# Kernel optimization log

Measured on AMD Instinct MI355X. Metric: run time of the kernel, lower is better.

Reference implementation:

```python
import jax, jax.numpy as jnp
import numpy as np

K_TAPS = 4

def batch_lsigf(h, S, x, b):
    """h: [Gout,E,K,Fin], S: [B,E,N,N], x: [B,Fin,N], b: [Gout,1] -> [B,Gout,N]."""
    Gout, E, K, Fin = h.shape
    B, _, _, N = S.shape
    xk = jnp.broadcast_to(x[:, None], (B, E, Fin, N))  # tap k=0
    taps = [xk]
    for _ in range(1, K):
        xk = jnp.matmul(xk, S)  # [B,E,Fin,N] @ [B,E,N,N]
        taps.append(xk)
    z = jnp.stack(taps, axis=2)  # [B,E,K,Fin,N]
    y = jnp.einsum('bekfn,gekf->bgn', z, h)
    if b is not None:
        y = y + b  # [Gout,1] broadcasts over nodes
    return y

def setup_inputs() -> dict:
    key = jax.random.key(0)
    ks = jax.random.split(key, 9)
    B, N = 16, 1024
    G = F = H = 128
    E, K = 1, K_TAPS
    sa = 1.0 / np.sqrt(G * K)
    sb = 1.0 / np.sqrt(H * K)
    return {
        'x': jax.random.normal(ks[0], (B, G, N), jnp.float32),
        'hidden': jax.random.normal(ks[1], (B, H, N), jnp.float32),
        'S': jax.random.normal(ks[2], (B, E, N, N), jnp.float32) / np.sqrt(N),
        'weight_A': jax.random.uniform(ks[3], (H, E, K, G), jnp.float32, -sa, sa),
        'weight_B': jax.random.uniform(ks[4], (H, E, K, H), jnp.float32, -sb, sb),
        'weight_D': jax.random.uniform(ks[5], (F, E, K, H), jnp.float32, -sb, sb),
        'bias_A': jax.random.uniform(ks[6], (H, 1), jnp.float32, -sa, sa),
        'bias_B': jax.random.uniform(ks[7], (H, 1), jnp.float32, -sb, sb),
        'bias_D': jax.random.uniform(ks[8], (F, 1), jnp.float32, -sb, sb),
    }

def reference(x, hidden, S, weight_A, weight_B, weight_D, bias_A, bias_B, bias_D):
    u_a = batch_lsigf(weight_A, S, x, bias_A)        # input path
    u_b = batch_lsigf(weight_B, S, hidden, bias_B)   # recurrent path
    h_next = jax.nn.relu(u_a + u_b)                  # new hidden state
    u = batch_lsigf(weight_D, S, h_next, bias_D)     # output projection
    return u
```

## Files before the change

kernel.cpp:

```cpp
#include <hip/hip_runtime.h>


typedef __attribute__((ext_vector_type(8))) short short8;
typedef __attribute__((ext_vector_type(4))) float floatx4;

#define AS1 __attribute__((address_space(1)))
#define AS3 __attribute__((address_space(3)))

__device__ __forceinline__ unsigned short f2bf(float f) {
  union { float f; unsigned u; } v; v.f = f;
  unsigned r = v.u + 0x7fffu + ((v.u >> 16) & 1u);
  return (unsigned short)(r >> 16);
}
__device__ __forceinline__ float bf2f(unsigned short b) {
  union { unsigned u; float f; } v; v.u = ((unsigned)b) << 16;
  return v.f;
}

__device__ __forceinline__ void gload16(const void* g, void* l) {
  __builtin_amdgcn_global_load_lds((const AS1 void*)g, (AS3 void*)l, 16, 0, 0);
}

template<int EPI, int KK>
__global__ __launch_bounds__(256, 2)
void gemm_bt(const unsigned short* __restrict__ A, long long aBatch, int lda,
             const unsigned short* __restrict__ Bt, long long bBatch, int ldb,
             const unsigned short* __restrict__ cinit, long long ciBatch,
             const float* __restrict__ bias,
             unsigned short* __restrict__ outb, long long obBatch,
             float* __restrict__ outf, long long ofBatch,
             unsigned short* __restrict__ mixv, long long mvBatch)
{
  constexpr int NT   = KK / 64;
  constexpr int MT   = (EPI == 3) ? 8 : 2;
  constexpr int PERB = 16 * MT;
  __shared__ unsigned short buf[4][128 * 64];

  const int wg  = blockIdx.x;
  const int xcd = wg & 7;
  const int idx = wg >> 3;
  const int b   = xcd * 2 + idx / PERB;
  const int r   = idx % PERB;
  const int n0  = (r & 15) * 64;
  const int m0  = (r >> 4) * 64;

  const int tid  = threadIdx.x;
  const int wave = tid >> 6;
  const int lane = tid & 63;
  const int wr   = (wave >> 1) * 32;
  const int wc   = (wave & 1) * 32;
  const int l15  = lane & 15;
  const int lhi  = lane >> 4;

  const unsigned short* Ab = A + (long long)b * aBatch;
  const unsigned short* Bb = Bt + (long long)b * bBatch;

  const unsigned short* src[4];
  int ldsoff[4];
  #pragma unroll
  for (int i = 0; i < 4; ++i) {
    const int u  = wave * 4 + i;
    const int rr = u * 8 + (lane >> 3);
    const int c8 = ((lane & 7) ^ (rr & 7)) * 8;
    src[i] = (rr < 64) ? Ab + (long long)(m0 + rr) * lda + c8
                       : Bb + (long long)(n0 + rr - 64) * ldb + c8;
    ldsoff[i] = u * 512;
  }
  auto stage = [&](int slot) {
    #pragma unroll
    for (int i = 0; i < 4; ++i) {
      gload16(src[i], &buf[slot][ldsoff[i]]);
      src[i] += 64;
    }
  };

  int aoff[2][2], boff[2][2];
  #pragma unroll
  for (int mi = 0; mi < 2; ++mi)
    #pragma unroll
    for (int kk = 0; kk < 2; ++kk) {
      const int rowa = wr + mi * 16 + l15;
      aoff[kk][mi] = rowa * 64 + (((kk * 4 + lhi) ^ (rowa & 7)) << 3);
      const int rowb = 64 + wc + mi * 16 + l15;
      boff[kk][mi] = rowb * 64 + (((kk * 4 + lhi) ^ (rowb & 7)) << 3);
    }

  floatx4 acc[2][2];
  #pragma unroll
  for (int mi = 0; mi < 2; ++mi)
    #pragma unroll
    for (int ni = 0; ni < 2; ++ni)
      acc[mi][ni] = (floatx4){0.f, 0.f, 0.f, 0.f};

  stage(0);
  if (NT > 1) stage(1);
  if (NT > 2) stage(2);

  #pragma unroll
  for (int t = 0; t < NT; ++t) {
    const int rem = NT - 1 - t;
    if (rem >= 2)      { asm volatile("s_waitcnt vmcnt(8)" ::: "memory"); }
    else if (rem == 1) { asm volatile("s_waitcnt vmcnt(4)" ::: "memory"); }
    else               { asm volatile("s_waitcnt vmcnt(0)" ::: "memory"); }
    __builtin_amdgcn_s_barrier();
    __builtin_amdgcn_sched_barrier(0);
    if (t + 3 < NT) stage((t + 3) & 3);

    const unsigned short* bp = &buf[t & 3][0];
    #pragma unroll
    for (int kk = 0; kk < 2; ++kk) {
      short8 af[2], bv[2];
      #pragma unroll
      for (int mi = 0; mi < 2; ++mi) af[mi] = *(const short8*)(bp + aoff[kk][mi]);
      #pragma unroll
      for (int ni = 0; ni < 2; ++ni) bv[ni] = *(const short8*)(bp + boff[kk][ni]);
      __builtin_amdgcn_s_setprio(1);
      #pragma unroll
      for (int mi = 0; mi < 2; ++mi)
        #pragma unroll
        for (int ni = 0; ni < 2; ++ni)
          acc[mi][ni] = __builtin_amdgcn_mfma_f32_16x16x32_bf16(af[mi], bv[ni], acc[mi][ni], 0, 0, 0);
      __builtin_amdgcn_s_setprio(0);
    }
  }

  if (EPI == 0) {
    const unsigned short* ci = cinit + (long long)b * ciBatch;
    unsigned short* ob = outb + (long long)b * obBatch;
    #pragma unroll
    for (int mi = 0; mi < 2; ++mi)
      #pragma unroll
      for (int ni = 0; ni < 2; ++ni)
        #pragma unroll
        for (int j = 0; j < 4; ++j) {
          const int row = m0 + wr + mi * 16 + lhi * 4 + j;
          const int col = n0 + wc + ni * 16 + l15;
          ob[(long long)row * 1024 + col] =
              f2bf(acc[mi][ni][j] + bf2f(ci[(long long)row * 1024 + col]));
        }
  } else if (EPI == 2) {
    const unsigned short* ci = cinit + (long long)b * ciBatch;
    float* of = outf + (long long)b * ofBatch;
    #pragma unroll
    for (int mi = 0; mi < 2; ++mi)
      #pragma unroll
      for (int ni = 0; ni < 2; ++ni)
        #pragma unroll
        for (int j = 0; j < 4; ++j) {
          const int row = m0 + wr + mi * 16 + lhi * 4 + j;
          const int col = n0 + wc + ni * 16 + l15;
          of[(long long)row * 1024 + col] =
              acc[mi][ni][j] + bf2f(ci[(long long)row * 1024 + col]);
        }
  } else if (EPI == 3) {
    #pragma unroll
    for (int mi = 0; mi < 2; ++mi)
      #pragma unroll
      for (int ni = 0; ni < 2; ++ni)
        #pragma unroll
        for (int j = 0; j < 4; ++j) {
          const int gr = m0 + wr + mi * 16 + lhi * 4 + j;
          const int kc = gr >> 7;
          const int rl = gr & 127;
          const int col = n0 + wc + ni * 16 + l15;
          unsigned short* dst = (kc == 3) ? (mixv + (long long)b * mvBatch)
                                          : (outb + (long long)b * obBatch + kc * (128 * 1024));
          float v = acc[mi][ni][j];
          if (kc == 0 && bias != nullptr) v += bias[rl];
          dst[(long long)rl * 1024 + col] = f2bf(v);
        }
  } else {
    const unsigned short* ci = cinit + (long long)b * ciBatch;
    __syncthreads();
    unsigned short (*tt)[72] = (unsigned short(*)[72])(&buf[0][0]);
    #pragma unroll
    for (int mi = 0; mi < 2; ++mi)
      #pragma unroll
      for (int ni = 0; ni < 2; ++ni)
        #pragma unroll
        for (int j = 0; j < 4; ++j) {
          const int rowl = wr + mi * 16 + lhi * 4 + j;
          const int coll = wc + ni * 16 + l15;
          float v = acc[mi][ni][j] +
                    bf2f(ci[(long long)(m0 + rowl) * 1024 + n0 + coll]);
          tt[coll][rowl] = f2bf(fmaxf(v, 0.f));
        }
    __syncthreads();
    unsigned short* ob = outb + (long long)b * obBatch;
    #pragma unroll
    for (int i = 0; i < 2; ++i) {
      const int flat = tid + i * 256;
      const int node = flat >> 3;
      const int seg  = flat & 7;
      *(short8*)(&ob[(long long)(n0 + node) * 128 + m0 + seg * 8]) =
          *(const short8*)(&tt[node][seg * 8]);
    }
  }
}

__global__ __launch_bounds__(256)
void prep_all(const float* __restrict__ x, const float* __restrict__ hid,
              const float* __restrict__ S,
              const float* __restrict__ wA, const float* __restrict__ wB,
              const float* __restrict__ wD,
              const float* __restrict__ bA, const float* __restrict__ bB,
              unsigned short* __restrict__ St, unsigned short* __restrict__ z0t,
              unsigned short* __restrict__ W1, unsigned short* __restrict__ W2,
              float* __restrict__ biasAB)
{
  __shared__ float t[64][65];
  const int wg  = blockIdx.x;
  const int tid = threadIdx.x;

  #pragma unroll
  for (int k = 0; k < 2; ++k) {
    const int i = wg * 512 + k * 256 + tid;
    if (i < 512 * 256) {
      const int row = i >> 8, g2 = i & 255;
      const int kk = row >> 7, h = row & 127;
      const float v = (g2 < 128) ? wA[(h * 4 + kk) * 128 + g2]
                                 : wB[(h * 4 + kk) * 128 + (g2 - 128)];
      W1[i] = f2bf(v);
    } else if (i < 512 * 256 + 512 * 128) {
      const int j = i - 512 * 256;
      const int row = j >> 7, h2 = j & 127;
      const int kk = row >> 7, f = row & 127;
      W2[j] = f2bf(wD[(f * 4 + kk) * 128 + h2]);
    } else if (i < 512 * 256 + 512 * 128 + 128) {
      const int l = i - 512 * 256 - 512 * 128;
      biasAB[l] = bA[l] + bB[l];
    }
  }

  const int b  = (wg & 7) * 2 + (wg >> 3) / 32;
  const int jj = (wg >> 3) % 32;
  const int tx = tid & 63;
  const int ty = tid >> 6;

  const float* Sb = S + (long long)b * (1024 * 1024);
  unsigned short* Stb = St + (long long)b * (1024 * 1024);
  for (int q = 0; q < 8; ++q) {
    const int tile = jj * 8 + q;
    const int c0 = (tile & 15) * 64, r0 = (tile >> 4) * 64;
    __syncthreads();
    #pragma unroll
    for (int i = 0; i < 64; i += 4)
      t[ty + i][tx] = Sb[(r0 + ty + i) * 1024 + c0 + tx];
    __syncthreads();
    #pragma unroll
    for (int i = 0; i < 64; i += 4)
      Stb[(long long)(c0 + ty + i) * 1024 + r0 + tx] = f2bf(t[tx][ty + i]);
  }

  unsigned short* zb = z0t + (long long)b * (1024 * 256);
  for (int q = 0; q < 2; ++q) {
    const int idx2 = jj * 2 + q;
    const int srch = idx2 >> 5;
    const int t2   = idx2 & 31;
    const int c0 = (t2 & 15) * 64, r0 = ((t2 >> 4) & 1) * 64;
    const float* sp = (srch ? hid : x) + (long long)b * (128 * 1024);
    __syncthreads();
    #pragma unroll
    for (int i = 0; i < 64; i += 4)
      t[ty + i][tx] = sp[(r0 + ty + i) * 1024 + c0 + tx];
    __syncthreads();
    #pragma unroll
    for (int i = 0; i < 64; i += 4)
      zb[(long long)(c0 + ty + i) * 256 + srch * 128 + r0 + tx] = f2bf(t[tx][ty + i]);
  }
}

extern "C" void kernel_launch(void* const* d_in, const int* in_sizes, int n_in,
                              void* d_out, int out_size, void* d_ws, size_t ws_size,
                              hipStream_t stream)
{
  const float* x   = (const float*)d_in[0];
  const float* hid = (const float*)d_in[1];
  const float* S   = (const float*)d_in[2];
  const float* wA  = (const float*)d_in[3];
  const float* wB  = (const float*)d_in[4];
  const float* wD  = (const float*)d_in[5];
  const float* bA  = (const float*)d_in[6];
  const float* bB  = (const float*)d_in[7];
  const float* bD  = (const float*)d_in[8];
  float* out = (float*)d_out;

  char* ws = (char*)d_ws;
  auto alloc = [&](size_t bytes) {
    char* p = ws;
    ws += (bytes + 255) & ~(size_t)255;
    return p;
  };
  unsigned short* St   = (unsigned short*)alloc(16ull * 1024 * 1024 * 2);
  unsigned short* z0t  = (unsigned short*)alloc(16ull * 1024 * 256 * 2);
  unsigned short* cini = (unsigned short*)alloc(16ull * 3 * 128 * 1024 * 2);
  unsigned short* vb0  = (unsigned short*)alloc(16ull * 128 * 1024 * 2);
  unsigned short* vb1  = (unsigned short*)alloc(16ull * 128 * 1024 * 2);
  unsigned short* hnt  = (unsigned short*)alloc(16ull * 1024 * 128 * 2);
  unsigned short* W1   = (unsigned short*)alloc(512 * 256 * 2);
  unsigned short* W2   = (unsigned short*)alloc(512 * 128 * 2);
  float*          bAB  = (float*)alloc(128 * 4);

  const long long NB  = 128 * 1024;
  const long long NB2 = 1024 * 128;
  const long long CI  = 3 * NB;
  const long long SB  = 1024 * 1024;

  prep_all<<<dim3(512), 256, 0, stream>>>(x, hid, S, wA, wB, wD, bA, bB,
                                          St, z0t, W1, W2, bAB);

  gemm_bt<3, 256><<<dim3(2048), 256, 0, stream>>>(W1, 0, 256, z0t, 1024 * 256, 256,
      nullptr, 0, bAB, cini, CI, nullptr, 0, vb0, NB);
  gemm_bt<0, 1024><<<dim3(512), 256, 0, stream>>>(vb0, NB, 1024, St, SB, 1024,
      cini + 2 * NB, CI, nullptr, vb1, NB, nullptr, 0, nullptr, 0);
  gemm_bt<0, 1024><<<dim3(512), 256, 0, stream>>>(vb1, NB, 1024, St, SB, 1024,
      cini + 1 * NB, CI, nullptr, vb0, NB, nullptr, 0, nullptr, 0);
  gemm_bt<4, 1024><<<dim3(512), 256, 0, stream>>>(vb0, NB, 1024, St, SB, 1024,
      cini, CI, nullptr, hnt, NB2, nullptr, 0, nullptr, 0);

  gemm_bt<3, 128><<<dim3(2048), 256, 0, stream>>>(W2, 0, 128, hnt, NB2, 128,
      nullptr, 0, bD, cini, CI, nullptr, 0, vb0, NB);
  gemm_bt<0, 1024><<<dim3(512), 256, 0, stream>>>(vb0, NB, 1024, St, SB, 1024,
      cini + 2 * NB, CI, nullptr, vb1, NB, nullptr, 0, nullptr, 0);
  gemm_bt<0, 1024><<<dim3(512), 256, 0, stream>>>(vb1, NB, 1024, St, SB, 1024,
      cini + 1 * NB, CI, nullptr, vb0, NB, nullptr, 0, nullptr, 0);
  gemm_bt<2, 1024><<<dim3(512), 256, 0, stream>>>(vb0, NB, 1024, St, SB, 1024,
      cini, CI, nullptr, nullptr, 0, out, NB, nullptr, 0);
}
```

Baseline: 107.3 us.

## Fuse S transpose into first mixing GEMM and use 2-wave tiles for S GEMMs

The S transpose/bf16 conversion moves out of the prep kernel into a combined kernel where every fifth block transposes S and the other blocks run the first weight-mixing GEMM, so the two independent jobs overlap. The 1024-K GEMMs against S now use 128-thread blocks with 2 waves, each holding a 32x64 accumulator tile with more MFMAs per LDS fragment load, and wait counts adjusted to match. This aims to remove the serial prep phase and cut LDS traffic per MFMA, at the cost of fewer waves per block for latency hiding, higher register pressure, and uneven block work in the fused kernel.

```diff
diff --git a/kernel.cpp b/kernel.cpp
--- a/kernel.cpp
+++ b/kernel.cpp
@@ -21,22 +21,24 @@
   __builtin_amdgcn_global_load_lds((const AS1 void*)g, (AS3 void*)l, 16, 0, 0);
 }
 
-template<int EPI, int KK>
-__global__ __launch_bounds__(256, 2)
-void gemm_bt(const unsigned short* __restrict__ A, long long aBatch, int lda,
-             const unsigned short* __restrict__ Bt, long long bBatch, int ldb,
-             const unsigned short* __restrict__ cinit, long long ciBatch,
-             const float* __restrict__ bias,
-             unsigned short* __restrict__ outb, long long obBatch,
-             float* __restrict__ outf, long long ofBatch,
-             unsigned short* __restrict__ mixv, long long mvBatch)
+template<int EPI, int KK, int NW>
+__device__ __forceinline__ void gemm_core(
+    const int wg, unsigned short (*buf)[128 * 64],
+    const unsigned short* __restrict__ A, long long aBatch, int lda,
+    const unsigned short* __restrict__ Bt, long long bBatch, int ldb,
+    const unsigned short* __restrict__ cinit, long long ciBatch,
+    const float* __restrict__ bias,
+    unsigned short* __restrict__ outb, long long obBatch,
+    float* __restrict__ outf, long long ofBatch,
+    unsigned short* __restrict__ mixv, long long mvBatch)
 {
   constexpr int NT   = KK / 64;
   constexpr int MT   = (EPI == 3) ? 8 : 2;
   constexpr int PERB = 16 * MT;
-  __shared__ unsigned short buf[4][128 * 64];
-
-  const int wg  = blockIdx.x;
+  constexpr int MI   = 2;
+  constexpr int NI   = (NW == 2) ? 4 : 2;
+  constexpr int LT   = (NW == 2) ? 8 : 4;
+
   const int xcd = wg & 7;
   const int idx = wg >> 3;
   const int b   = xcd * 2 + idx / PERB;
@@ -47,19 +49,19 @@
   const int tid  = threadIdx.x;
   const int wave = tid >> 6;
   const int lane = tid & 63;
-  const int wr   = (wave >> 1) * 32;
-  const int wc   = (wave & 1) * 32;
+  const int wr   = (NW == 4) ? (wave >> 1) * 32 : wave * 32;
+  const int wc   = (NW == 4) ? (wave & 1) * 32 : 0;
   const int l15  = lane & 15;
   const int lhi  = lane >> 4;
 
   const unsigned short* Ab = A + (long long)b * aBatch;
   const unsigned short* Bb = Bt + (long long)b * bBatch;
 
-  const unsigned short* src[4];
-  int ldsoff[4];
-  #pragma unroll
-  for (int i = 0; i < 4; ++i) {
-    const int u  = wave * 4 + i;
+  const unsigned short* src[LT];
+  int ldsoff[LT];
+  #pragma unroll
+  for (int i = 0; i < LT; ++i) {
+    const int u  = wave * LT + i;
     const int rr = u * 8 + (lane >> 3);
     const int c8 = ((lane & 7) ^ (rr & 7)) * 8;
     src[i] = (rr < 64) ? Ab + (long long)(m0 + rr) * lda + c8
@@ -68,28 +70,32 @@
   }
   auto stage = [&](int slot) {
     #pragma unroll
-    for (int i = 0; i < 4; ++i) {
+    for (int i = 0; i < LT; ++i) {
       gload16(src[i], &buf[slot][ldsoff[i]]);
       src[i] += 64;
     }
   };
 
-  int aoff[2][2], boff[2][2];
-  #pragma unroll
-  for (int mi = 0; mi < 2; ++mi)
-    #pragma unroll
-    for (int kk = 0; kk < 2; ++kk) {
+  int aoff[2][MI], boff[2][NI];
+  #pragma unroll
+  for (int kk = 0; kk < 2; ++kk) {
+    #pragma unroll
+    for (int mi = 0; mi < MI; ++mi) {
       const int rowa = wr + mi * 16 + l15;
       aoff[kk][mi] = rowa * 64 + (((kk * 4 + lhi) ^ (rowa & 7)) << 3);
-      const int rowb = 64 + wc + mi * 16 + l15;
-      boff[kk][mi] = rowb * 64 + (((kk * 4 + lhi) ^ (rowb & 7)) << 3);
-    }
-
-  floatx4 acc[2][2];
-  #pragma unroll
-  for (int mi = 0; mi < 2; ++mi)
-    #pragma unroll
-    for (int ni = 0; ni < 2; ++ni)
+    }
+    #pragma unroll
+    for (int ni = 0; ni < NI; ++ni) {
+      const int rowb = 64 + wc + ni * 16 + l15;
+      boff[kk][ni] = rowb * 64 + (((kk * 4 + lhi) ^ (rowb & 7)) << 3);
+    }
+  }
+
+  floatx4 acc[MI][NI];
+  #pragma unroll
+  for (int mi = 0; mi < MI; ++mi)
+    #pragma unroll
+    for (int ni = 0; ni < NI; ++ni)
       acc[mi][ni] = (floatx4){0.f, 0.f, 0.f, 0.f};
 
   stage(0);
@@ -99,9 +105,15 @@
   #pragma unroll
   for (int t = 0; t < NT; ++t) {
     const int rem = NT - 1 - t;
-    if (rem >= 2)      { asm volatile("s_waitcnt vmcnt(8)" ::: "memory"); }
-    else if (rem == 1) { asm volatile("s_waitcnt vmcnt(4)" ::: "memory"); }
-    else               { asm volatile("s_waitcnt vmcnt(0)" ::: "memory"); }
+    if (rem >= 2) {
+      if constexpr (LT == 4) asm volatile("s_waitcnt vmcnt(8)"  ::: "memory");
+      else                   asm volatile("s_waitcnt vmcnt(16)" ::: "memory");
+    } else if (rem == 1) {
+      if constexpr (LT == 4) asm volatile("s_waitcnt vmcnt(4)"  ::: "memory");
+      else                   asm volatile("s_waitcnt vmcnt(8)"  ::: "memory");
+    } else {
+      asm volatile("s_waitcnt vmcnt(0)" ::: "memory");
+    }
     __builtin_amdgcn_s_barrier();
     __builtin_amdgcn_sched_barrier(0);
     if (t + 3 < NT) stage((t + 3) & 3);
@@ -109,16 +121,16 @@
     const unsigned short* bp = &buf[t & 3][0];
     #pragma unroll
     for (int kk = 0; kk < 2; ++kk) {
-      short8 af[2], bv[2];
-      #pragma unroll
-      for (int mi = 0; mi < 2; ++mi) af[mi] = *(const short8*)(bp + aoff[kk][mi]);
-      #pragma unroll
-      for (int ni = 0; ni < 2; ++ni) bv[ni] = *(const short8*)(bp + boff[kk][ni]);
+      short8 af[MI], bv[NI];
+      #pragma unroll
+      for (int mi = 0; mi < MI; ++mi) af[mi] = *(const short8*)(bp + aoff[kk][mi]);
+      #pragma unroll
+      for (int ni = 0; ni < NI; ++ni) bv[ni] = *(const short8*)(bp + boff[kk][ni]);
       __builtin_amdgcn_s_setprio(1);
       #pragma unroll
-      for (int mi = 0; mi < 2; ++mi)
-        #pragma unroll
-        for (int ni = 0; ni < 2; ++ni)
+      for (int mi = 0; mi < MI; ++mi)
+        #pragma unroll
+        for (int ni = 0; ni < NI; ++ni)
           acc[mi][ni] = __builtin_amdgcn_mfma_f32_16x16x32_bf16(af[mi], bv[ni], acc[mi][ni], 0, 0, 0);
       __builtin_amdgcn_s_setprio(0);
     }
@@ -128,9 +140,9 @@
     const unsigned short* ci = cinit + (long long)b * ciBatch;
     unsigned short* ob = outb + (long long)b * obBatch;
     #pragma unroll
-    for (int mi = 0; mi < 2; ++mi)
-      #pragma unroll
-      for (int ni = 0; ni < 2; ++ni)
+    for (int mi = 0; mi < MI; ++mi)
+      #pragma unroll
+      for (int ni = 0; ni < NI; ++ni)
         #pragma unroll
         for (int j = 0; j < 4; ++j) {
           const int row = m0 + wr + mi * 16 + lhi * 4 + j;
@@ -142,9 +154,9 @@
     const unsigned short* ci = cinit + (long long)b * ciBatch;
     float* of = outf + (long long)b * ofBatch;
     #pragma unroll
-    for (int mi = 0; mi < 2; ++mi)
-      #pragma unroll
-      for (int ni = 0; ni < 2; ++ni)
+    for (int mi = 0; mi < MI; ++mi)
+      #pragma unroll
+      for (int ni = 0; ni < NI; ++ni)
         #pragma unroll
         for (int j = 0; j < 4; ++j) {
           const int row = m0 + wr + mi * 16 + lhi * 4 + j;
@@ -154,9 +166,9 @@
         }
   } else if (EPI == 3) {
     #pragma unroll
-    for (int mi = 0; mi < 2; ++mi)
-      #pragma unroll
-      for (int ni = 0; ni < 2; ++ni)
+    for (int mi = 0; mi < MI; ++mi)
+      #pragma unroll
+      for (int ni = 0; ni < NI; ++ni)
         #pragma unroll
         for (int j = 0; j < 4; ++j) {
           const int gr = m0 + wr + mi * 16 + lhi * 4 + j;
@@ -174,9 +186,9 @@
     __syncthreads();
     unsigned short (*tt)[72] = (unsigned short(*)[72])(&buf[0][0]);
     #pragma unroll
-    for (int mi = 0; mi < 2; ++mi)
-      #pragma unroll
-      for (int ni = 0; ni < 2; ++ni)
+    for (int mi = 0; mi < MI; ++mi)
+      #pragma unroll
+      for (int ni = 0; ni < NI; ++ni)
         #pragma unroll
         for (int j = 0; j < 4; ++j) {
           const int rowl = wr + mi * 16 + lhi * 4 + j;
@@ -188,8 +200,8 @@
     __syncthreads();
     unsigned short* ob = outb + (long long)b * obBatch;
     #pragma unroll
-    for (int i = 0; i < 2; ++i) {
-      const int flat = tid + i * 256;
+    for (int i = 0; i < 512 / (NW * 64); ++i) {
+      const int flat = tid + i * (NW * 64);
       const int node = flat >> 3;
       const int seg  = flat & 7;
       *(short8*)(&ob[(long long)(n0 + node) * 128 + m0 + seg * 8]) =
@@ -198,15 +210,70 @@
   }
 }
 
+template<int EPI, int KK, int NW>
+__global__ __launch_bounds__(NW * 64, 2)
+void gemm_bt(const unsigned short* __restrict__ A, long long aBatch, int lda,
+             const unsigned short* __restrict__ Bt, long long bBatch, int ldb,
+             const unsigned short* __restrict__ cinit, long long ciBatch,
+             const float* __restrict__ bias,
+             unsigned short* __restrict__ outb, long long obBatch,
+             float* __restrict__ outf, long long ofBatch,
+             unsigned short* __restrict__ mixv, long long mvBatch)
+{
+  __shared__ unsigned short buf[4][128 * 64];
+  gemm_core<EPI, KK, NW>(blockIdx.x, buf, A, aBatch, lda, Bt, bBatch, ldb,
+                         cinit, ciBatch, bias, outb, obBatch, outf, ofBatch,
+                         mixv, mvBatch);
+}
+
+__global__ __launch_bounds__(256, 2)
+void fused_S_mix1(const float* __restrict__ S, unsigned short* __restrict__ St,
+                  const unsigned short* __restrict__ W1,
+                  const unsigned short* __restrict__ z0t,
+                  const float* __restrict__ bAB,
+                  unsigned short* __restrict__ cini,
+                  unsigned short* __restrict__ vb0)
+{
+  __shared__ unsigned short buf[4][128 * 64];
+  const int bid = blockIdx.x;
+  if (bid % 5 == 0) {
+    const int sidx = bid / 5;
+    const int b  = (sidx & 7) * 2 + (sidx >> 3) / 32;
+    const int jj = (sidx >> 3) % 32;
+    const int tid = threadIdx.x;
+    const int tx = tid & 63;
+    const int ty = tid >> 6;
+    float (*t)[65] = (float(*)[65])(&buf[0][0]);
+    const float* Sb = S + (long long)b * (1024 * 1024);
+    unsigned short* Stb = St + (long long)b * (1024 * 1024);
+    for (int q = 0; q < 8; ++q) {
+      const int tile = jj * 8 + q;
+      const int c0 = (tile & 15) * 64, r0 = (tile >> 4) * 64;
+      __syncthreads();
+      #pragma unroll
+      for (int i = 0; i < 64; i += 4)
+        t[ty + i][tx] = Sb[(long long)(r0 + ty + i) * 1024 + c0 + tx];
+      __syncthreads();
+      #pragma unroll
+      for (int i = 0; i < 64; i += 4)
+        Stb[(long long)(c0 + ty + i) * 1024 + r0 + tx] = f2bf(t[tx][ty + i]);
+    }
+  } else {
+    const int midx = bid - 1 - bid / 5;
+    gemm_core<3, 256, 4>(midx, buf, W1, 0, 256, z0t, 1024 * 256, 256,
+                         nullptr, 0, bAB, cini, 3LL * 128 * 1024,
+                         nullptr, 0, vb0, 128 * 1024);
+  }
+}
+
 __global__ __launch_bounds__(256)
-void prep_all(const float* __restrict__ x, const float* __restrict__ hid,
-              const float* __restrict__ S,
-              const float* __restrict__ wA, const float* __restrict__ wB,
-              const float* __restrict__ wD,
-              const float* __restrict__ bA, const float* __restrict__ bB,
-              unsigned short* __restrict__ St, unsigned short* __restrict__ z0t,
-              unsigned short* __restrict__ W1, unsigned short* __restrict__ W2,
-              float* __restrict__ biasAB)
+void prep_z(const float* __restrict__ x, const float* __restrict__ hid,
+            const float* __restrict__ wA, const float* __restrict__ wB,
+            const float* __restrict__ wD,
+            const float* __restrict__ bA, const float* __restrict__ bB,
+            unsigned short* __restrict__ z0t,
+            unsigned short* __restrict__ W1, unsigned short* __restrict__ W2,
+            float* __restrict__ biasAB)
 {
   __shared__ float t[64][65];
   const int wg  = blockIdx.x;
@@ -237,21 +304,6 @@
   const int tx = tid & 63;
   const int ty = tid >> 6;
 
-  const float* Sb = S + (long long)b * (1024 * 1024);
-  unsigned short* Stb = St + (long long)b * (1024 * 1024);
-  for (int q = 0; q < 8; ++q) {
-    const int tile = jj * 8 + q;
-    const int c0 = (tile & 15) * 64, r0 = (tile >> 4) * 64;
-    __syncthreads();
-    #pragma unroll
-    for (int i = 0; i < 64; i += 4)
-      t[ty + i][tx] = Sb[(r0 + ty + i) * 1024 + c0 + tx];
-    __syncthreads();
-    #pragma unroll
-    for (int i = 0; i < 64; i += 4)
-      Stb[(long long)(c0 + ty + i) * 1024 + r0 + tx] = f2bf(t[tx][ty + i]);
-  }
-
   unsigned short* zb = z0t + (long long)b * (1024 * 256);
   for (int q = 0; q < 2; ++q) {
     const int idx2 = jj * 2 + q;
@@ -262,7 +314,7 @@
     __syncthreads();
     #pragma unroll
     for (int i = 0; i < 64; i += 4)
-      t[ty + i][tx] = sp[(r0 + ty + i) * 1024 + c0 + tx];
+      t[ty + i][tx] = sp[(long long)(r0 + ty + i) * 1024 + c0 + tx];
     __syncthreads();
     #pragma unroll
     for (int i = 0; i < 64; i += 4)
@@ -306,24 +358,24 @@
   const long long CI  = 3 * NB;
   const long long SB  = 1024 * 1024;
 
-  prep_all<<<dim3(512), 256, 0, stream>>>(x, hid, S, wA, wB, wD, bA, bB,
-                                          St, z0t, W1, W2, bAB);
-
-  gemm_bt<3, 256><<<dim3(2048), 256, 0, stream>>>(W1, 0, 256, z0t, 1024 * 256, 256,
-      nullptr, 0, bAB, cini, CI, nullptr, 0, vb0, NB);
-  gemm_bt<0, 1024><<<dim3(512), 256, 0, stream>>>(vb0, NB, 1024, St, SB, 1024,
+  prep_z<<<dim3(512), 256, 0, stream>>>(x, hid, wA, wB, wD, bA, bB,
+                                        z0t, W1, W2, bAB);
+
+  fused_S_mix1<<<dim3(2560), 256, 0, stream>>>(S, St, W1, z0t, bAB, cini, vb0);
+
+  gemm_bt<0, 1024, 2><<<dim3(512), 128, 0, stream>>>(vb0, NB, 1024, St, SB, 1024,
       cini + 2 * NB, CI, nullptr, vb1, NB, nullptr, 0, nullptr, 0);
-  gemm_bt<0, 1024><<<dim3(512), 256, 0, stream>>>(vb1, NB, 1024, St, SB, 1024,
+  gemm_bt<0, 1024, 2><<<dim3(512), 128, 0, stream>>>(vb1, NB, 1024, St, SB, 1024,
       cini + 1 * NB, CI, nullptr, vb0, NB, nullptr, 0, nullptr, 0);
-  gemm_bt<4, 1024><<<dim3(512), 256, 0, stream>>>(vb0, NB, 1024, St, SB, 1024,
+  gemm_bt<4, 1024, 2><<<dim3(512), 128, 0, stream>>>(vb0, NB, 1024, St, SB, 1024,
       cini, CI, nullptr, hnt, NB2, nullptr, 0, nullptr, 0);
 
-  gemm_bt<3, 128><<<dim3(2048), 256, 0, stream>>>(W2, 0, 128, hnt, NB2, 128,
+  gemm_bt<3, 128, 4><<<dim3(2048), 256, 0, stream>>>(W2, 0, 128, hnt, NB2, 128,
       nullptr, 0, bD, cini, CI, nullptr, 0, vb0, NB);
-  gemm_bt<0, 1024><<<dim3(512), 256, 0, stream>>>(vb0, NB, 1024, St, SB, 1024,
+  gemm_bt<0, 1024, 2><<<dim3(512), 128, 0, stream>>>(vb0, NB, 1024, St, SB, 1024,
       cini + 2 * NB, CI, nullptr, vb1, NB, nullptr, 0, nullptr, 0);
-  gemm_bt<0, 1024><<<dim3(512), 256, 0, stream>>>(vb1, NB, 1024, St, SB, 1024,
+  gemm_bt<0, 1024, 2><<<dim3(512), 128, 0, stream>>>(vb1, NB, 1024, St, SB, 1024,
       cini + 1 * NB, CI, nullptr, vb0, NB, nullptr, 0, nullptr, 0);
-  gemm_bt<2, 1024><<<dim3(512), 256, 0, stream>>>(vb0, NB, 1024, St, SB, 1024,
+  gemm_bt<2, 1024, 2><<<dim3(512), 128, 0, stream>>>(vb0, NB, 1024, St, SB, 1024,
       cini, CI, nullptr, nullptr, 0, out, NB, nullptr, 0);
 }
```

Result: slower. 111.4 us (+3.8%).

## Pre-pack S into MFMA fragment layout and load B operands straight to registers

Applied to the files above, without the earlier changes.

The prep kernel now writes S in a packed bf16 layout that matches the MFMA B-fragment order. The propagation GEMM then loads B fragments straight from global memory into registers with a three-deep register prefetch, and only A is staged through LDS. This halves LDS traffic and LDS footprint per block and drops the B-side LDS reads. The cost is more VGPR pressure, hand-tuned vmcnt waits that are fragile, and B reuse across waves now going through cache instead of shared memory. The mix GEMM is split into its own kernel with an unchanged algorithm.

```diff
diff --git a/kernel.cpp b/kernel.cpp
--- a/kernel.cpp
+++ b/kernel.cpp
@@ -3,6 +3,7 @@
 
 typedef __attribute__((ext_vector_type(8))) short short8;
 typedef __attribute__((ext_vector_type(4))) float floatx4;
+typedef __attribute__((ext_vector_type(4))) int   intx4;
 
 #define AS1 __attribute__((address_space(1)))
 #define AS3 __attribute__((address_space(3)))
@@ -21,26 +22,26 @@
   __builtin_amdgcn_global_load_lds((const AS1 void*)g, (AS3 void*)l, 16, 0, 0);
 }
 
-template<int EPI, int KK>
+#define LOADB(dst, p) \
+  asm volatile("global_load_dwordx4 %0, %1, off" : "=v"(dst) : "v"(p) : "memory")
+
+union BVU { intx4 i; short8 s; };
+
+template<int EPI>
 __global__ __launch_bounds__(256, 2)
-void gemm_bt(const unsigned short* __restrict__ A, long long aBatch, int lda,
-             const unsigned short* __restrict__ Bt, long long bBatch, int ldb,
-             const unsigned short* __restrict__ cinit, long long ciBatch,
-             const float* __restrict__ bias,
-             unsigned short* __restrict__ outb, long long obBatch,
-             float* __restrict__ outf, long long ofBatch,
-             unsigned short* __restrict__ mixv, long long mvBatch)
+void prop_gemm(const unsigned short* __restrict__ A,
+               const unsigned short* __restrict__ Bp,
+               const unsigned short* __restrict__ cinit, long long ciBatch,
+               unsigned short* __restrict__ outb, long long obBatch,
+               float* __restrict__ outf)
 {
-  constexpr int NT   = KK / 64;
-  constexpr int MT   = (EPI == 3) ? 8 : 2;
-  constexpr int PERB = 16 * MT;
-  __shared__ unsigned short buf[4][128 * 64];
+  __shared__ unsigned short buf[4][64 * 64];
 
   const int wg  = blockIdx.x;
   const int xcd = wg & 7;
   const int idx = wg >> 3;
-  const int b   = xcd * 2 + idx / PERB;
-  const int r   = idx % PERB;
+  const int b   = xcd * 2 + idx / 32;
+  const int r   = idx % 32;
   const int n0  = (r & 15) * 64;
   const int m0  = (r >> 4) * 64;
 
@@ -52,37 +53,34 @@
   const int l15  = lane & 15;
   const int lhi  = lane >> 4;
 
-  const unsigned short* Ab = A + (long long)b * aBatch;
-  const unsigned short* Bb = Bt + (long long)b * bBatch;
-
-  const unsigned short* src[4];
-  int ldsoff[4];
-  #pragma unroll
-  for (int i = 0; i < 4; ++i) {
-    const int u  = wave * 4 + i;
-    const int rr = u * 8 + (lane >> 3);
-    const int c8 = ((lane & 7) ^ (rr & 7)) * 8;
-    src[i] = (rr < 64) ? Ab + (long long)(m0 + rr) * lda + c8
-                       : Bb + (long long)(n0 + rr - 64) * ldb + c8;
-    ldsoff[i] = u * 512;
-  }
-  auto stage = [&](int slot) {
-    #pragma unroll
-    for (int i = 0; i < 4; ++i) {
-      gload16(src[i], &buf[slot][ldsoff[i]]);
-      src[i] += 64;
-    }
+  const unsigned short* Ab = A + (long long)b * (128 * 1024);
+  const unsigned short* Bb = Bp + (long long)b * (1 << 20);
+
+  const unsigned short* asrc[2];
+  #pragma unroll
+  for (int i = 0; i < 2; ++i) {
+    const int q  = tid + i * 256;
+    const int rr = q >> 3;
+    const int c8 = ((q & 7) ^ (rr & 7)) * 8;
+    asrc[i] = Ab + (long long)(m0 + rr) * 1024 + c8;
+  }
+  auto stageA = [&](int slot, int sidx) {
+    #pragma unroll
+    for (int i = 0; i < 2; ++i)
+      gload16(asrc[i] + sidx * 64, &buf[slot][(tid + i * 256) * 8]);
   };
 
-  int aoff[2][2], boff[2][2];
-  #pragma unroll
-  for (int mi = 0; mi < 2; ++mi)
-    #pragma unroll
-    for (int kk = 0; kk < 2; ++kk) {
+  const int nt0 = (n0 >> 4) + (wave & 1) * 2;
+  const unsigned short* bp0 = Bb + ((long long)nt0 * 32 * 64 + lane) * 8;
+  const unsigned short* bp1 = bp0 + 32 * 64 * 8;
+
+  int aoff[2][2];
+  #pragma unroll
+  for (int kk = 0; kk < 2; ++kk)
+    #pragma unroll
+    for (int mi = 0; mi < 2; ++mi) {
       const int rowa = wr + mi * 16 + l15;
       aoff[kk][mi] = rowa * 64 + (((kk * 4 + lhi) ^ (rowa & 7)) << 3);
-      const int rowb = 64 + wc + mi * 16 + l15;
-      boff[kk][mi] = rowb * 64 + (((kk * 4 + lhi) ^ (rowb & 7)) << 3);
     }
 
   floatx4 acc[2][2];
@@ -92,36 +90,68 @@
     for (int ni = 0; ni < 2; ++ni)
       acc[mi][ni] = (floatx4){0.f, 0.f, 0.f, 0.f};
 
-  stage(0);
-  if (NT > 1) stage(1);
-  if (NT > 2) stage(2);
-
-  #pragma unroll
-  for (int t = 0; t < NT; ++t) {
-    const int rem = NT - 1 - t;
-    if (rem >= 2)      { asm volatile("s_waitcnt vmcnt(8)" ::: "memory"); }
-    else if (rem == 1) { asm volatile("s_waitcnt vmcnt(4)" ::: "memory"); }
-    else               { asm volatile("s_waitcnt vmcnt(0)" ::: "memory"); }
-    __builtin_amdgcn_s_barrier();
+  intx4 breg[3][2][2];
+
+  stageA(0, 0); stageA(1, 1); stageA(2, 2);
+  LOADB(breg[1][0][0], bp0);        LOADB(breg[1][0][1], bp1);
+  LOADB(breg[1][1][0], bp0 + 512);  LOADB(breg[1][1][1], bp1 + 512);
+  LOADB(breg[2][0][0], bp0 + 1024); LOADB(breg[2][0][1], bp1 + 1024);
+  LOADB(breg[2][1][0], bp0 + 1536); LOADB(breg[2][1][1], bp1 + 1536);
+  bp0 += 2048; bp1 += 2048;
+
+  asm volatile("s_waitcnt vmcnt(12)" ::: "memory");
+  __builtin_amdgcn_s_barrier();
+
+  #pragma unroll
+  for (int s = 0; s < 16; ++s) {
     __builtin_amdgcn_sched_barrier(0);
-    if (t + 3 < NT) stage((t + 3) & 3);
-
-    const unsigned short* bp = &buf[t & 3][0];
-    #pragma unroll
-    for (int kk = 0; kk < 2; ++kk) {
-      short8 af[2], bv[2];
-      #pragma unroll
-      for (int mi = 0; mi < 2; ++mi) af[mi] = *(const short8*)(bp + aoff[kk][mi]);
-      #pragma unroll
-      for (int ni = 0; ni < 2; ++ni) bv[ni] = *(const short8*)(bp + boff[kk][ni]);
+    if (s + 3 < 16) stageA((s + 3) & 3, s + 3);
+    if (s < 14) {
+      const int ld = s % 3;
+      LOADB(breg[ld][0][0], bp0);       LOADB(breg[ld][0][1], bp1);
+      LOADB(breg[ld][1][0], bp0 + 512); LOADB(breg[ld][1][1], bp1 + 512);
+      bp0 += 1024; bp1 += 1024;
+    }
+
+    const unsigned short* sp = &buf[s & 3][0];
+    short8 af0[2], af1[2];
+    #pragma unroll
+    for (int mi = 0; mi < 2; ++mi) af0[mi] = *(const short8*)(sp + aoff[0][mi]);
+    #pragma unroll
+    for (int mi = 0; mi < 2; ++mi) af1[mi] = *(const short8*)(sp + aoff[1][mi]);
+
+    const int cs = (s + 1) % 3;
+    if (s == 0)       asm volatile("s_waitcnt vmcnt(12)" ::: "memory");
+    else if (s <= 12) asm volatile("s_waitcnt vmcnt(14)" ::: "memory");
+    else if (s == 13) asm volatile("s_waitcnt vmcnt(12)" ::: "memory");
+    else if (s == 14) asm volatile("s_waitcnt vmcnt(6)"  ::: "memory");
+    else              asm volatile("s_waitcnt vmcnt(2)"  ::: "memory");
+    __builtin_amdgcn_sched_barrier(0);
+    {
+      BVU u0, u1; u0.i = breg[cs][0][0]; u1.i = breg[cs][0][1];
       __builtin_amdgcn_s_setprio(1);
-      #pragma unroll
-      for (int mi = 0; mi < 2; ++mi)
-        #pragma unroll
-        for (int ni = 0; ni < 2; ++ni)
-          acc[mi][ni] = __builtin_amdgcn_mfma_f32_16x16x32_bf16(af[mi], bv[ni], acc[mi][ni], 0, 0, 0);
+      acc[0][0] = __builtin_amdgcn_mfma_f32_16x16x32_bf16(af0[0], u0.s, acc[0][0], 0, 0, 0);
+      acc[0][1] = __builtin_amdgcn_mfma_f32_16x16x32_bf16(af0[0], u1.s, acc[0][1], 0, 0, 0);
+      acc[1][0] = __builtin_amdgcn_mfma_f32_16x16x32_bf16(af0[1], u0.s, acc[1][0], 0, 0, 0);
+      acc[1][1] = __builtin_amdgcn_mfma_f32_16x16x32_bf16(af0[1], u1.s, acc[1][1], 0, 0, 0);
       __builtin_amdgcn_s_setprio(0);
     }
+    if (s == 0)       asm volatile("s_waitcnt vmcnt(10)" ::: "memory");
+    else if (s <= 12) asm volatile("s_waitcnt vmcnt(12)" ::: "memory");
+    else if (s == 13) asm volatile("s_waitcnt vmcnt(10)" ::: "memory");
+    else if (s == 14) asm volatile("s_waitcnt vmcnt(4)"  ::: "memory");
+    else              asm volatile("s_waitcnt vmcnt(0)"  ::: "memory");
+    __builtin_amdgcn_sched_barrier(0);
+    {
+      BVU u0, u1; u0.i = breg[cs][1][0]; u1.i = breg[cs][1][1];
+      __builtin_amdgcn_s_setprio(1);
+      acc[0][0] = __builtin_amdgcn_mfma_f32_16x16x32_bf16(af1[0], u0.s, acc[0][0], 0, 0, 0);
+      acc[0][1] = __builtin_amdgcn_mfma_f32_16x16x32_bf16(af1[0], u1.s, acc[0][1], 0, 0, 0);
+      acc[1][0] = __builtin_amdgcn_mfma_f32_16x16x32_bf16(af1[1], u0.s, acc[1][0], 0, 0, 0);
+      acc[1][1] = __builtin_amdgcn_mfma_f32_16x16x32_bf16(af1[1], u1.s, acc[1][1], 0, 0, 0);
+      __builtin_amdgcn_s_setprio(0);
+    }
+    if (s < 15) __builtin_amdgcn_s_barrier();
   }
 
   if (EPI == 0) {
@@ -140,7 +170,7 @@
         }
   } else if (EPI == 2) {
     const unsigned short* ci = cinit + (long long)b * ciBatch;
-    float* of = outf + (long long)b * ofBatch;
+    float* of = outf + (long long)b * (128 * 1024);
     #pragma unroll
     for (int mi = 0; mi < 2; ++mi)
       #pragma unroll
@@ -151,23 +181,6 @@
           const int col = n0 + wc + ni * 16 + l15;
           of[(long long)row * 1024 + col] =
               acc[mi][ni][j] + bf2f(ci[(long long)row * 1024 + col]);
-        }
-  } else if (EPI == 3) {
-    #pragma unroll
-    for (int mi = 0; mi < 2; ++mi)
-      #pragma unroll
-      for (int ni = 0; ni < 2; ++ni)
-        #pragma unroll
-        for (int j = 0; j < 4; ++j) {
-          const int gr = m0 + wr + mi * 16 + lhi * 4 + j;
-          const int kc = gr >> 7;
-          const int rl = gr & 127;
-          const int col = n0 + wc + ni * 16 + l15;
-          unsigned short* dst = (kc == 3) ? (mixv + (long long)b * mvBatch)
-                                          : (outb + (long long)b * obBatch + kc * (128 * 1024));
-          float v = acc[mi][ni][j];
-          if (kc == 0 && bias != nullptr) v += bias[rl];
-          dst[(long long)rl * 1024 + col] = f2bf(v);
         }
   } else {
     const unsigned short* ci = cinit + (long long)b * ciBatch;
@@ -198,13 +211,134 @@
   }
 }
 
+template<int KK>
+__global__ __launch_bounds__(256, 2)
+void mix_gemm(const unsigned short* __restrict__ W, int lda,
+              const unsigned short* __restrict__ Bt, long long bBatch, int ldb,
+              const float* __restrict__ bias,
+              unsigned short* __restrict__ cini,
+              unsigned short* __restrict__ mixv)
+{
+  constexpr int NT = KK / 64;
+  __shared__ unsigned short buf[4][128 * 64];
+
+  const int wg  = blockIdx.x;
+  const int xcd = wg & 7;
+  const int idx = wg >> 3;
+  const int b   = xcd * 2 + idx / 128;
+  const int r   = idx % 128;
+  const int n0  = (r & 15) * 64;
+  const int m0  = (r >> 4) * 64;
+
+  const int tid  = threadIdx.x;
+  const int wave = tid >> 6;
+  const int lane = tid & 63;
+  const int wr   = (wave >> 1) * 32;
+  const int wc   = (wave & 1) * 32;
+  const int l15  = lane & 15;
+  const int lhi  = lane >> 4;
+
+  const unsigned short* Bb = Bt + (long long)b * bBatch;
+
+  const unsigned short* src[4];
+  int ldsoff[4];
+  #pragma unroll
+  for (int i = 0; i < 4; ++i) {
+    const int u  = wave * 4 + i;
+    const int q  = u * 64 + lane;
+    const int rr = q >> 3;
+    const int c8 = ((q & 7) ^ (rr & 7)) * 8;
+    src[i] = (rr < 64) ? W + (long long)(m0 + rr) * lda + c8
+                       : Bb + (long long)(n0 + rr - 64) * ldb + c8;
+    ldsoff[i] = u * 512;
+  }
+  auto stage = [&](int slot) {
+    #pragma unroll
+    for (int i = 0; i < 4; ++i) {
+      gload16(src[i], &buf[slot][ldsoff[i]]);
+      src[i] += 64;
+    }
+  };
+
+  int aoff[2][2], boff[2][2];
+  #pragma unroll
+  for (int kk = 0; kk < 2; ++kk) {
+    #pragma unroll
+    for (int mi = 0; mi < 2; ++mi) {
+      const int rowa = wr + mi * 16 + l15;
+      aoff[kk][mi] = rowa * 64 + (((kk * 4 + lhi) ^ (rowa & 7)) << 3);
+    }
+    #pragma unroll
+    for (int ni = 0; ni < 2; ++ni) {
+      const int rowb = 64 + wc + ni * 16 + l15;
+      boff[kk][ni] = rowb * 64 + (((kk * 4 + lhi) ^ (rowb & 7)) << 3);
+    }
+  }
+
+  floatx4 acc[2][2];
+  #pragma unroll
+  for (int mi = 0; mi < 2; ++mi)
+    #pragma unroll
+    for (int ni = 0; ni < 2; ++ni)
+      acc[mi][ni] = (floatx4){0.f, 0.f, 0.f, 0.f};
+
+  stage(0);
+  if (NT > 1) stage(1);
+  if (NT > 2) stage(2);
+
+  #pragma unroll
+  for (int t = 0; t < NT; ++t) {
+    const int rem = NT - 1 - t;
+    if (rem >= 2)      asm volatile("s_waitcnt vmcnt(8)" ::: "memory");
+    else if (rem == 1) asm volatile("s_waitcnt vmcnt(4)" ::: "memory");
+    else               asm volatile("s_waitcnt vmcnt(0)" ::: "memory");
+    __builtin_amdgcn_s_barrier();
+    __builtin_amdgcn_sched_barrier(0);
+    if (t + 3 < NT) stage((t + 3) & 3);
+
+    const unsigned short* bp = &buf[t & 3][0];
+    #pragma unroll
+    for (int kk = 0; kk < 2; ++kk) {
+      short8 af[2], bv[2];
+      #pragma unroll
+      for (int mi = 0; mi < 2; ++mi) af[mi] = *(const short8*)(bp + aoff[kk][mi]);
+      #pragma unroll
+      for (int ni = 0; ni < 2; ++ni) bv[ni] = *(const short8*)(bp + boff[kk][ni]);
+      __builtin_amdgcn_s_setprio(1);
+      #pragma unroll
+      for (int mi = 0; mi < 2; ++mi)
+        #pragma unroll
+        for (int ni = 0; ni < 2; ++ni)
+          acc[mi][ni] = __builtin_amdgcn_mfma_f32_16x16x32_bf16(af[mi], bv[ni], acc[mi][ni], 0, 0, 0);
+      __builtin_amdgcn_s_setprio(0);
+    }
+  }
+
+  #pragma unroll
+  for (int mi = 0; mi < 2; ++mi)
+    #pragma unroll
+    for (int ni = 0; ni < 2; ++ni)
+      #pragma unroll
+      for (int j = 0; j < 4; ++j) {
+        const int gr = m0 + wr + mi * 16 + lhi * 4 + j;
+        const int kc = gr >> 7;
+        const int rl = gr & 127;
+        const int col = n0 + wc + ni * 16 + l15;
+        unsigned short* dst = (kc == 3) ? (mixv + (long long)b * (128 * 1024))
+                                        : (cini + (long long)b * (3LL * 128 * 1024) + kc * (128 * 1024));
+        float v = acc[mi][ni][j];
+        if (kc == 0) v += bias[rl];
+        dst[(long long)rl * 1024 + col] = f2bf(v);
+      }
+}
+
 __global__ __launch_bounds__(256)
 void prep_all(const float* __restrict__ x, const float* __restrict__ hid,
               const float* __restrict__ S,
               const float* __restrict__ wA, const float* __restrict__ wB,
               const float* __restrict__ wD,
               const float* __restrict__ bA, const float* __restrict__ bB,
-              unsigned short* __restrict__ St, unsigned short* __restrict__ z0t,
+              unsigned short* __restrict__ Bpack, unsigned short* __restrict__ z0t,
               unsigned short* __restrict__ W1, unsigned short* __restrict__ W2,
               float* __restrict__ biasAB)
 {
@@ -238,18 +372,35 @@
   const int ty = tid >> 6;
 
   const float* Sb = S + (long long)b * (1024 * 1024);
-  unsigned short* Stb = St + (long long)b * (1024 * 1024);
+  unsigned short* Bpb = Bpack + (long long)b * (1 << 20);
   for (int q = 0; q < 8; ++q) {
     const int tile = jj * 8 + q;
-    const int c0 = (tile & 15) * 64, r0 = (tile >> 4) * 64;
+    const int c0 = (tile & 15) * 64;
+    const int r0 = (tile >> 4) * 64;
     __syncthreads();
     #pragma unroll
     for (int i = 0; i < 64; i += 4)
-      t[ty + i][tx] = Sb[(r0 + ty + i) * 1024 + c0 + tx];
-    __syncthreads();
-    #pragma unroll
-    for (int i = 0; i < 64; i += 4)
-      Stb[(long long)(c0 + ty + i) * 1024 + r0 + tx] = f2bf(t[tx][ty + i]);
+      t[ty + i][tx] = Sb[(long long)(r0 + ty + i) * 1024 + c0 + tx];
+    __syncthreads();
+    #pragma unroll
+    for (int w2 = 0; w2 < 2; ++w2) {
+      const int u  = tid + w2 * 256;
+      const int p  = u >> 6;
+      const int l  = u & 63;
+      const int nl = (p & 3) * 16 + (l & 15);
+      const int kl = (p >> 2) * 32 + (l >> 4) * 8;
+      unsigned vv[4];
+      #pragma unroll
+      for (int e = 0; e < 4; ++e) {
+        const unsigned lo = f2bf(t[kl + 2 * e][nl]);
+        const unsigned hi = f2bf(t[kl + 2 * e + 1][nl]);
+        vv[e] = lo | (hi << 16);
+      }
+      const long long nt_g = (c0 >> 4) + (p & 3);
+      const long long ks_g = (r0 >> 5) + (p >> 2);
+      uint4* dst = (uint4*)(Bpb + (nt_g * 32 + ks_g) * 512 + l * 8);
+      *dst = (uint4){vv[0], vv[1], vv[2], vv[3]};
+    }
   }
 
   unsigned short* zb = z0t + (long long)b * (1024 * 256);
@@ -262,7 +413,7 @@
     __syncthreads();
     #pragma unroll
     for (int i = 0; i < 64; i += 4)
-      t[ty + i][tx] = sp[(r0 + ty + i) * 1024 + c0 + tx];
+      t[ty + i][tx] = sp[(long long)(r0 + ty + i) * 1024 + c0 + tx];
     __syncthreads();
     #pragma unroll
     for (int i = 0; i < 64; i += 4)
@@ -291,7 +442,7 @@
     ws += (bytes + 255) & ~(size_t)255;
     return p;
   };
-  unsigned short* St   = (unsigned short*)alloc(16ull * 1024 * 1024 * 2);
+  unsigned short* Bpack = (unsigned short*)alloc(16ull * (1 << 20) * 2);
   unsigned short* z0t  = (unsigned short*)alloc(16ull * 1024 * 256 * 2);
   unsigned short* cini = (unsigned short*)alloc(16ull * 3 * 128 * 1024 * 2);
   unsigned short* vb0  = (unsigned short*)alloc(16ull * 128 * 1024 * 2);
@@ -304,26 +455,25 @@
   const long long NB  = 128 * 1024;
   const long long NB2 = 1024 * 128;
   const long long CI  = 3 * NB;
-  const long long SB  = 1024 * 1024;
 
   prep_all<<<dim3(512), 256, 0, stream>>>(x, hid, S, wA, wB, wD, bA, bB,
-                                          St, z0t, W1, W2, bAB);
-
-  gemm_bt<3, 256><<<dim3(2048), 256, 0, stream>>>(W1, 0, 256, z0t, 1024 * 256, 256,
-      nullptr, 0, bAB, cini, CI, nullptr, 0, vb0, NB);
-  gemm_bt<0, 1024><<<dim3(512), 256, 0, stream>>>(vb0, NB, 1024, St, SB, 1024,
-      cini + 2 * NB, CI, nullptr, vb1, NB, nullptr, 0, nullptr, 0);
-  gemm_bt<0, 1024><<<dim3(512), 256, 0, stream>>>(vb1, NB, 1024, St, SB, 1024,
-      cini + 1 * NB, CI, nullptr, vb0, NB, nullptr, 0, nullptr, 0);
-  gemm_bt<4, 1024><<<dim3(512), 256, 0, stream>>>(vb0, NB, 1024, St, SB, 1024,
-      cini, CI, nullptr, hnt, NB2, nullptr, 0, nullptr, 0);
-
-  gemm_bt<3, 128><<<dim3(2048), 256, 0, stream>>>(W2, 0, 128, hnt, NB2, 128,
-      nullptr, 0, bD, cini, CI, nullptr, 0, vb0, NB);
-  gemm_bt<0, 1024><<<dim3(512), 256, 0, stream>>>(vb0, NB, 1024, St, SB, 1024,
-      cini + 2 * NB, CI, nullptr, vb1, NB, nullptr, 0, nullptr, 0);
-  gemm_bt<0, 1024><<<dim3(512), 256, 0, stream>>>(vb1, NB, 1024, St, SB, 1024,
-      cini + 1 * NB, CI, nullptr, vb0, NB, nullptr, 0, nullptr, 0);
-  gemm_bt<2, 1024><<<dim3(512), 256, 0, stream>>>(vb0, NB, 1024, St, SB, 1024,
-      cini, CI, nullptr, nullptr, 0, out, NB, nullptr, 0);
-}
+                                          Bpack, z0t, W1, W2, bAB);
+
+  mix_gemm<256><<<dim3(2048), 256, 0, stream>>>(W1, 256, z0t, 1024 * 256, 256,
+      bAB, cini, vb0);
+  prop_gemm<0><<<dim3(512), 256, 0, stream>>>(vb0, Bpack, cini + 2 * NB, CI,
+      vb1, NB, nullptr);
+  prop_gemm<0><<<dim3(512), 256, 0, stream>>>(vb1, Bpack, cini + 1 * NB, CI,
+      vb0, NB, nullptr);
+  prop_gemm<4><<<dim3(512), 256, 0, stream>>>(vb0, Bpack, cini, CI,
+      hnt, NB2, nullptr);
+
+  mix_gemm<128><<<dim3(2048), 256, 0, stream>>>(W2, 128, hnt, NB2, 128,
+      bD, cini, vb0);
+  prop_gemm<0><<<dim3(512), 256, 0, stream>>>(vb0, Bpack, cini + 2 * NB, CI,
+      vb1, NB, nullptr);
+  prop_gemm<0><<<dim3(512), 256, 0, stream>>>(vb1, Bpack, cini + 1 * NB, CI,
+      vb0, NB, nullptr);
+  prop_gemm<2><<<dim3(512), 256, 0, stream>>>(vb0, Bpack, cini, CI,
+      nullptr, 0, out);
+}
```

New measurement: 113.1 us. 5.4% more time.
